# Optimization experiments

Hardware: AMD Instinct MI355X
Metric: run time of the kernel (lower is better)

## Reference

```python
import jax, jax.numpy as jnp
import numpy as np

B, C, P, E, M, H, K = 1024, 8192, 3, 64, 128, 16, 8
SCALE = 0.05
EPS = 1e-12  # tf.math.l2_normalize epsilon


def setup_inputs() -> dict:
    key = jax.random.key(0)
    ks = jax.random.split(key, 16)
    return {
        'pools': jax.random.uniform(ks[0], (B, C), dtype=jnp.float32),            # dense stand-in for SparseTensor batch_pools
        'metapaths': jax.random.uniform(ks[1], (P, C, C), dtype=jnp.float32),     # card-card metapath matrices
        'card_embeddings': jax.random.normal(ks[2], (C, E), dtype=jnp.float32) * SCALE,
        'mp_kernels': jax.random.normal(ks[3], (P, E, M), dtype=jnp.float32) * SCALE,
        'mp_biases': jnp.zeros((P, M, 1), dtype=jnp.float32),
        'Wq': jax.random.normal(ks[4], (M, H, K), dtype=jnp.float32) * SCALE,
        'bq': jnp.zeros((H, K), dtype=jnp.float32),
        'Wk': jax.random.normal(ks[5], (M, H, K), dtype=jnp.float32) * SCALE,
        'bk': jnp.zeros((H, K), dtype=jnp.float32),
        'Wv': jax.random.normal(ks[6], (M, H, K), dtype=jnp.float32) * SCALE,
        'bv': jnp.zeros((H, K), dtype=jnp.float32),
        'Wo': jax.random.normal(ks[7], (H, K, M), dtype=jnp.float32) * SCALE,
        'bo': jnp.zeros((M,), dtype=jnp.float32),
        'pool_kernel': jax.random.normal(ks[8], (M, E), dtype=jnp.float32) * SCALE,
        'pool_bias': jnp.zeros((E,), dtype=jnp.float32),
    }


def _l2_normalize(x, axis):
    # matches tf.math.l2_normalize: x / sqrt(max(sum(x^2), eps))
    sq = jnp.sum(jnp.square(x), axis=axis, keepdims=True)
    return x * jax.lax.rsqrt(jnp.maximum(sq, EPS))


def reference(pools, metapaths, card_embeddings, mp_kernels, mp_biases,
              Wq, bq, Wk, bk, Wv, bv, Wo, bo, pool_kernel, pool_bias):
    # --- MetapathEmbed layers, vectorized over the P metapaths ---
    # path_card_embeddings: act(einsum('ce,em->mc') + bias) -> (P, M, C)
    path_card = jax.nn.silu(jnp.einsum('ce,pem->pmc', card_embeddings, mp_kernels) + mp_biases)
    # path_card_matrix: einsum('mc,cd->dm') -> (P, C, M)
    pcm = jnp.einsum('pmc,pcd->pdm', path_card, metapaths)
    # sparse_dense_matmul(batch_pools, path_card_matrix); stack over metapaths -> (B, P, M)
    x = jnp.einsum('bd,pdm->bpm', pools, pcm)

    # --- keras MultiHeadAttention(query=x, value=x) ---
    q = jnp.einsum('bpm,mhk->bphk', x, Wq) + bq
    k = jnp.einsum('bpm,mhk->bphk', x, Wk) + bk
    v = jnp.einsum('bpm,mhk->bphk', x, Wv) + bv
    scores = jnp.einsum('bphk,bqhk->bhpq', q, k) / np.float32(np.sqrt(K))
    attn = jax.nn.softmax(scores, axis=-1)
    o = jnp.einsum('bhpq,bqhk->bphk', attn, v)
    attended = jnp.einsum('bphk,hkm->bpm', o, Wo) + bo  # (B, P, M)

    # --- pooling head ---
    pre_pool = jnp.sum(attended, axis=1)                       # (B, M)
    pool_embeds = jnp.einsum('bm,me->be', pre_pool, pool_kernel) + pool_bias
    norm_pool = _l2_normalize(pool_embeds, axis=1)             # (B, E)
    norm_cards = _l2_normalize(card_embeddings, axis=1)        # (C, E)
    return (jnp.einsum('be,ce->bc', norm_pool, norm_cards) + 1.0) / 2.0
```

## Files before the change

kernel.cpp:

```cpp
#include <hip/hip_runtime.h>
#include <hip/hip_bf16.h>

typedef unsigned int uint;
typedef unsigned short ushort;
typedef float f32x4 __attribute__((ext_vector_type(4)));
typedef short s16x8 __attribute__((ext_vector_type(8)));
typedef int i32x4 __attribute__((ext_vector_type(4)));
typedef uint u32x2 __attribute__((ext_vector_type(2)));

#define C_DIM 8192
#define B_DIM 1024
#define P_DIM 3
#define E_DIM 64
#define M_DIM 128

#define PCA_OFF   0ull
#define PART_OFF  15728640ull
#define PCMH_OFF  66060288ull
#define PCML_OFF  72351744ull
#define XPART_OFF PART_OFF
#define NPOOL_OFF 78643200ull
#define NCARD_OFF 78774272ull

__device__ __forceinline__ uint bf16_rne(float f) {
  uint u = __builtin_bit_cast(uint, f);
  return (u + 0x7fffu + ((u >> 16) & 1u)) >> 16;
}
__device__ __forceinline__ float bf16_to_f32(uint b) {
  return __builtin_bit_cast(float, b << 16);
}
__device__ __forceinline__ uint pk2(float a, float b) {
  float2 t; t.x = a; t.y = b;
  __hip_bfloat162 h2 = __float22bfloat162_rn(t);
  uint r;
  __builtin_memcpy(&r, &h2, 4);
  return r;
}

__global__ __launch_bounds__(256) void k1_pathcard(
    const float* __restrict__ cardemb, const float* __restrict__ mpk,
    const float* __restrict__ mpbias, ushort* __restrict__ pcA) {
  __shared__ float ce_l[64 * 68];
  const int tid = threadIdx.x;
  const int cb = blockIdx.x;
  const int p  = blockIdx.y;
  for (int r = 0; r < 16; ++r) {
    int i = r * 256 + tid;
    int row = i >> 6, col = i & 63;
    ce_l[row * 68 + col] = cardemb[(size_t)(cb * 64 + row) * 64 + col];
  }
  __syncthreads();
  const int m = tid & 127;
  const int chalf = tid >> 7;
  float kr[64];
#pragma unroll
  for (int e = 0; e < 64; ++e) kr[e] = mpk[(size_t)p * E_DIM * M_DIM + e * M_DIM + m];
  const float bias = mpbias[p * M_DIM + m];
  for (int cl0 = 0; cl0 < 32; ++cl0) {
    int cl = chalf * 32 + cl0;
    float acc = bias;
#pragma unroll
    for (int e = 0; e < 64; ++e) acc += ce_l[cl * 68 + e] * kr[e];
    float s = acc / (1.0f + expf(-acc));
    uint hb = bf16_rne(s);
    uint lb = bf16_rne(s - bf16_to_f32(hb));
    int c = cb * 64 + cl;
    int kt = c >> 5, kl = c & 31;
    size_t off = ((size_t)(p * 256 + kt) * 20480 + (size_t)m * 80 + (size_t)kl * 2) >> 1;
    pcA[off] = (ushort)hb;
    pcA[off + 5120] = (ushort)lb;
  }
}

__global__ __launch_bounds__(256, 3) void k2_big(
    const float* __restrict__ mp, const ushort* __restrict__ pcA,
    float* __restrict__ partial) {
  __shared__ char smem[32768];
  const int tid = threadIdx.x;
  int lin = blockIdx.x + 64 * (blockIdx.y + 4 * blockIdx.z);
  int swz = (lin & 7) * 96 + (lin >> 3);
  const int dt = swz & 63, q = (swz >> 6) & 3, p = swz >> 8;
  const int lane = tid & 63, wid = tid >> 6;
  const int wr = wid >> 1, wc = wid & 1;
  const int r16 = lane & 15, g4 = lane >> 4;
  const float* mpb = mp + (size_t)p * C_DIM * C_DIM + (size_t)dt * 128;
  const char* pcb = (const char*)pcA + (size_t)(p * 256 + q * 64) * 20480;
  const int sd = tid & 127, skh = tid >> 7;
  const int fc = ((sd ^ (sd >> 2)) & 3) << 4;
  const int fr = ((r16 ^ (r16 >> 2)) & 3) << 4;

  f32x4 acc[4][4];
#pragma unroll
  for (int i = 0; i < 4; ++i)
#pragma unroll
    for (int j = 0; j < 4; ++j) acc[i][j] = (f32x4){0.f, 0.f, 0.f, 0.f};

  auto loadB = [&](int t, float* br) {
    int c0 = q * 2048 + t * 32;
#pragma unroll
    for (int ii = 0; ii < 2; ++ii) {
      const float* rp = mpb + (size_t)(c0 + ii * 16 + skh * 8) * C_DIM + sd;
#pragma unroll
      for (int j = 0; j < 8; ++j) br[ii * 8 + j] = rp[(size_t)j * C_DIM];
    }
  };
  auto writeB = [&](const float* br, int buf) {
    char* bb = smem + buf * 16384;
#pragma unroll
    for (int ii = 0; ii < 2; ++ii) {
      uint hw[4], lw[4];
#pragma unroll
      for (int k2 = 0; k2 < 4; ++k2) {
        float v0 = br[ii * 8 + k2 * 2], v1 = br[ii * 8 + k2 * 2 + 1];
        uint h = pk2(v0, v1);
        float h0 = __builtin_bit_cast(float, h << 16);
        float h1 = __builtin_bit_cast(float, h & 0xffff0000u);
        hw[k2] = h;
        lw[k2] = pk2(v0 - h0, v1 - h1);
      }
      int off = sd * 64 + ((((ii * 2 + skh) << 4)) ^ fc);
      *(i32x4*)(bb + off) = (i32x4){(int)hw[0], (int)hw[1], (int)hw[2], (int)hw[3]};
      *(i32x4*)(bb + 8192 + off) = (i32x4){(int)lw[0], (int)lw[1], (int)lw[2], (int)lw[3]};
    }
  };
  auto compute = [&](int t, int buf) {
    const char* At = pcb + (size_t)t * 20480;
    const char* Bb = smem + buf * 16384;
    s16x8 ah[4], al[4], bh[4], bl[4];
#pragma unroll
    for (int i = 0; i < 4; ++i) {
      int off = (wr * 64 + i * 16 + r16) * 80 + g4 * 16;
      ah[i] = *(const s16x8*)(At + off);
      al[i] = *(const s16x8*)(At + 10240 + off);
    }
#pragma unroll
    for (int j = 0; j < 4; ++j) {
      int off = (wc * 64 + j * 16 + r16) * 64 + ((g4 << 4) ^ fr);
      bh[j] = *(const s16x8*)(Bb + off);
      bl[j] = *(const s16x8*)(Bb + 8192 + off);
    }
#pragma unroll
    for (int i = 0; i < 4; ++i)
#pragma unroll
      for (int j = 0; j < 4; ++j) {
        acc[i][j] = __builtin_amdgcn_mfma_f32_16x16x32_bf16(ah[i], bh[j], acc[i][j], 0, 0, 0);
        acc[i][j] = __builtin_amdgcn_mfma_f32_16x16x32_bf16(ah[i], bl[j], acc[i][j], 0, 0, 0);
        acc[i][j] = __builtin_amdgcn_mfma_f32_16x16x32_bf16(al[i], bh[j], acc[i][j], 0, 0, 0);
      }
  };

  float brA[16], brB[16];
  loadB(0, brA);
  loadB(1, brB);
  writeB(brA, 0);
  asm volatile("s_waitcnt lgkmcnt(0)" ::: "memory");
  __builtin_amdgcn_s_barrier();
  __builtin_amdgcn_sched_barrier(0);

#define K2S(T, BRL, BRW, TAIL)                                                \
  {                                                                           \
    if ((T) < 62) loadB((T) + 2, BRL);                                        \
    compute((T), (T) & 1);                                                    \
    if (!(TAIL)) {                                                            \
      writeB(BRW, ((T) + 1) & 1);                                             \
      asm volatile("s_waitcnt lgkmcnt(0)" ::: "memory");                      \
      __builtin_amdgcn_s_barrier();                                           \
      __builtin_amdgcn_sched_barrier(0);                                      \
    }                                                                         \
  }

  for (int t2 = 0; t2 < 32; ++t2) {
    int t = 2 * t2;
    K2S(t, brA, brB, false);
    K2S(t + 1, brB, brA, (t2 == 31));
  }
#undef K2S

  float* part = partial + (size_t)(q * 3 + p) * M_DIM * C_DIM + (size_t)dt * 128;
#pragma unroll
  for (int i = 0; i < 4; ++i)
#pragma unroll
    for (int j = 0; j < 4; ++j)
#pragma unroll
      for (int r = 0; r < 4; ++r)
        part[(size_t)(wr * 64 + i * 16 + g4 * 4 + r) * C_DIM + (wc * 64 + j * 16 + r16)] =
            acc[i][j][r];
}

__global__ __launch_bounds__(256) void k2b_reduce(const float* __restrict__ p0,
                                                  ushort* __restrict__ oh,
                                                  ushort* __restrict__ ol) {
  size_t i = (size_t)blockIdx.x * 256 + threadIdx.x;
  f32x4 a = *(const f32x4*)(p0 + i * 4);
  f32x4 b = *(const f32x4*)(p0 + 3145728ull + i * 4);
  f32x4 c = *(const f32x4*)(p0 + 6291456ull + i * 4);
  f32x4 d = *(const f32x4*)(p0 + 9437184ull + i * 4);
  f32x4 s = (a + b) + (c + d);
  uint h[2], l[2];
#pragma unroll
  for (int k = 0; k < 2; ++k) {
    float v0 = s[k * 2], v1 = s[k * 2 + 1];
    uint hh = pk2(v0, v1);
    float h0 = __builtin_bit_cast(float, hh << 16);
    float h1 = __builtin_bit_cast(float, hh & 0xffff0000u);
    h[k] = hh;
    l[k] = pk2(v0 - h0, v1 - h1);
  }
  *(u32x2*)(oh + i * 4) = (u32x2){h[0], h[1]};
  *(u32x2*)(ol + i * 4) = (u32x2){l[0], l[1]};
}

__global__ __launch_bounds__(256, 2) void k3_x(const float* __restrict__ pools,
                                               const ushort* __restrict__ pcmh,
                                               const ushort* __restrict__ pcml,
                                               float* __restrict__ xpart) {
  const int tid = threadIdx.x;
  const int bt = blockIdx.x, ks = blockIdx.y;
  const int lane = tid & 63, w = tid >> 6;
  const int r16 = lane & 15, g4 = lane >> 4;
  const int rowbase = bt * 32;
  f32x4 acc[2][6];
#pragma unroll
  for (int i = 0; i < 2; ++i)
#pragma unroll
    for (int j = 0; j < 6; ++j) acc[i][j] = (f32x4){0.f, 0.f, 0.f, 0.f};

  f32x4 pv0[2], pv1[2];
#pragma unroll
  for (int i = 0; i < 2; ++i) {
    const float* ap = pools + (size_t)(rowbase + i * 16 + r16) * C_DIM + ks * 512 + g4 * 8;
    pv0[i] = *(const f32x4*)ap;
    pv1[i] = *(const f32x4*)(ap + 4);
  }

  for (int t = 0; t < 16; ++t) {
    int d0 = ks * 512 + t * 32 + g4 * 8;
    s16x8 ah[2], al[2];
#pragma unroll
    for (int i = 0; i < 2; ++i) {
      i32x4 hw, lw;
#pragma unroll
      for (int k2 = 0; k2 < 4; ++k2) {
        float x0 = (k2 < 2) ? pv0[i][k2 * 2] : pv1[i][(k2 - 2) * 2];
        float x1 = (k2 < 2) ? pv0[i][k2 * 2 + 1] : pv1[i][(k2 - 2) * 2 + 1];
        uint h = pk2(x0, x1);
        float h0 = __builtin_bit_cast(float, h << 16);
        float h1 = __builtin_bit_cast(float, h & 0xffff0000u);
        hw[k2] = (int)h;
        lw[k2] = (int)pk2(x0 - h0, x1 - h1);
      }
      ah[i] = __builtin_bit_cast(s16x8, hw);
      al[i] = __builtin_bit_cast(s16x8, lw);
    }
    if (t < 15) {
#pragma unroll
      for (int i = 0; i < 2; ++i) {
        const float* ap =
            pools + (size_t)(rowbase + i * 16 + r16) * C_DIM + d0 + 32;
        pv0[i] = *(const f32x4*)ap;
        pv1[i] = *(const f32x4*)(ap + 4);
      }
    }
#pragma unroll
    for (int j = 0; j < 6; ++j) {
      int col = w * 96 + j * 16 + r16;
      size_t boff = (size_t)col * C_DIM + d0;
      s16x8 bh = *(const s16x8*)(pcmh + boff);
      s16x8 bl = *(const s16x8*)(pcml + boff);
#pragma unroll
      for (int i = 0; i < 2; ++i) {
        acc[i][j] = __builtin_amdgcn_mfma_f32_16x16x32_bf16(ah[i], bh, acc[i][j], 0, 0, 0);
        acc[i][j] = __builtin_amdgcn_mfma_f32_16x16x32_bf16(ah[i], bl, acc[i][j], 0, 0, 0);
        acc[i][j] = __builtin_amdgcn_mfma_f32_16x16x32_bf16(al[i], bh, acc[i][j], 0, 0, 0);
      }
    }
  }
#pragma unroll
  for (int i = 0; i < 2; ++i)
#pragma unroll
    for (int j = 0; j < 6; ++j)
#pragma unroll
      for (int r = 0; r < 4; ++r) {
        int row = rowbase + i * 16 + g4 * 4 + r;
        int col = w * 96 + j * 16 + r16;
        int p = col >> 7, m = col & 127;
        xpart[((size_t)(ks * B_DIM + row) * 3 + p) * M_DIM + m] = acc[i][j][r];
      }
}

__global__ __launch_bounds__(128) void k4_attn(
    const float* __restrict__ xpart, const float* __restrict__ Wq,
    const float* __restrict__ bq, const float* __restrict__ Wk,
    const float* __restrict__ bk, const float* __restrict__ Wv,
    const float* __restrict__ bv, const float* __restrict__ Wo,
    const float* __restrict__ bo, const float* __restrict__ pk,
    const float* __restrict__ pb, ushort* __restrict__ npool) {
  __shared__ float xs[3 * 128], qa[3 * 128], ka[3 * 128], va[3 * 128], oa[3 * 128], pp[128];
  const int t = threadIdx.x;
  const int b = blockIdx.x;
#pragma unroll
  for (int p = 0; p < 3; ++p) {
    float v = 0.f;
    for (int ks = 0; ks < 16; ++ks)
      v += xpart[((size_t)(ks * B_DIM + b) * 3 + p) * M_DIM + t];
    xs[p * 128 + t] = v;
  }
  __syncthreads();
  float qv[3], kv[3], vv[3];
#pragma unroll
  for (int p = 0; p < 3; ++p) { qv[p] = bq[t]; kv[p] = bk[t]; vv[p] = bv[t]; }
  for (int m = 0; m < 128; ++m) {
    float wq = Wq[m * 128 + t], wk = Wk[m * 128 + t], wv = Wv[m * 128 + t];
#pragma unroll
    for (int p = 0; p < 3; ++p) {
      float xv = xs[p * 128 + m];
      qv[p] += xv * wq;
      kv[p] += xv * wk;
      vv[p] += xv * wv;
    }
  }
#pragma unroll
  for (int p = 0; p < 3; ++p) {
    qa[p * 128 + t] = qv[p];
    ka[p * 128 + t] = kv[p];
    va[p * 128 + t] = vv[p];
  }
  __syncthreads();
  const int h = t >> 3;
  float w[3][3];
#pragma unroll
  for (int p = 0; p < 3; ++p) {
    float s[3];
#pragma unroll
    for (int qq = 0; qq < 3; ++qq) {
      float d = 0.f;
#pragma unroll
      for (int kk = 0; kk < 8; ++kk)
        d += qa[p * 128 + h * 8 + kk] * ka[qq * 128 + h * 8 + kk];
      s[qq] = d / 2.8284271247461903f;
    }
    float mx = fmaxf(s[0], fmaxf(s[1], s[2]));
    float e0 = expf(s[0] - mx), e1 = expf(s[1] - mx), e2 = expf(s[2] - mx);
    float inv = 1.0f / (e0 + e1 + e2);
    w[p][0] = e0 * inv; w[p][1] = e1 * inv; w[p][2] = e2 * inv;
  }
#pragma unroll
  for (int p = 0; p < 3; ++p) {
    float o = w[p][0] * va[0 * 128 + t] + w[p][1] * va[1 * 128 + t] + w[p][2] * va[2 * 128 + t];
    oa[p * 128 + t] = o;
  }
  __syncthreads();
  float pre = 3.0f * bo[t];
#pragma unroll
  for (int p = 0; p < 3; ++p)
    for (int hk = 0; hk < 128; ++hk) pre += oa[p * 128 + hk] * Wo[hk * 128 + t];
  pp[t] = pre;
  __syncthreads();
  if (t < 64) {
    float pe = pb[t];
    for (int m = 0; m < 128; ++m) pe += pp[m] * pk[m * 64 + t];
    float ss = pe * pe;
#pragma unroll
    for (int off = 32; off; off >>= 1) ss += __shfl_xor(ss, off, 64);
    float rs = 1.0f / sqrtf(fmaxf(ss, 1e-12f));
    npool[b * 64 + t] = (ushort)bf16_rne(pe * rs);
  }
}

__global__ __launch_bounds__(256) void k4b_ncard(const float* __restrict__ ce,
                                                 ushort* __restrict__ ncard) {
  const int t = threadIdx.x;
  const int r = blockIdx.x * 4 + (t >> 6);
  const int lane = t & 63;
  float v = ce[(size_t)r * 64 + lane];
  float ss = v * v;
#pragma unroll
  for (int off = 32; off; off >>= 1) ss += __shfl_xor(ss, off, 64);
  float rs = 1.0f / sqrtf(fmaxf(ss, 1e-12f));
  ncard[(size_t)r * 64 + lane] = (ushort)bf16_rne(v * rs);
}

__global__ __launch_bounds__(256, 2) void k5_out(const ushort* __restrict__ np_,
                                                 const ushort* __restrict__ nc,
                                                 float* __restrict__ out) {
  const int tid = threadIdx.x;
  const int bt = blockIdx.x, ct = blockIdx.y;
  const int lane = tid & 63, wid = tid >> 6;
  const int wr = wid >> 1, wc = wid & 1;
  const int r16 = lane & 15, g4 = lane >> 4;
  f32x4 acc[4][4];
#pragma unroll
  for (int i = 0; i < 4; ++i)
#pragma unroll
    for (int j = 0; j < 4; ++j) acc[i][j] = (f32x4){0.f, 0.f, 0.f, 0.f};
#pragma unroll
  for (int ks = 0; ks < 2; ++ks) {
    int e0 = ks * 32 + g4 * 8;
    s16x8 af[4], bf_[4];
#pragma unroll
    for (int i = 0; i < 4; ++i)
      af[i] = *(const s16x8*)(np_ + (size_t)(bt * 128 + wr * 64 + i * 16 + r16) * 64 + e0);
#pragma unroll
    for (int j = 0; j < 4; ++j)
      bf_[j] = *(const s16x8*)(nc + (size_t)(ct * 128 + wc * 64 + j * 16 + r16) * 64 + e0);
#pragma unroll
    for (int i = 0; i < 4; ++i)
#pragma unroll
      for (int j = 0; j < 4; ++j)
        acc[i][j] = __builtin_amdgcn_mfma_f32_16x16x32_bf16(af[i], bf_[j], acc[i][j], 0, 0, 0);
  }
#pragma unroll
  for (int i = 0; i < 4; ++i)
#pragma unroll
    for (int j = 0; j < 4; ++j)
#pragma unroll
      for (int r = 0; r < 4; ++r) {
        int row = bt * 128 + wr * 64 + i * 16 + g4 * 4 + r;
        int col = ct * 128 + wc * 64 + j * 16 + r16;
        out[(size_t)row * C_DIM + col] = (acc[i][j][r] + 1.0f) * 0.5f;
      }
}

extern "C" void kernel_launch(void* const* d_in, const int* in_sizes, int n_in,
                              void* d_out, int out_size, void* d_ws, size_t ws_size,
                              hipStream_t stream) {
  const float* pools = (const float*)d_in[0];
  const float* metapaths = (const float*)d_in[1];
  const float* cardemb = (const float*)d_in[2];
  const float* mpk = (const float*)d_in[3];
  const float* mpbias = (const float*)d_in[4];
  const float* Wq = (const float*)d_in[5];
  const float* bq = (const float*)d_in[6];
  const float* Wk = (const float*)d_in[7];
  const float* bk = (const float*)d_in[8];
  const float* Wv = (const float*)d_in[9];
  const float* bv = (const float*)d_in[10];
  const float* Wo = (const float*)d_in[11];
  const float* bo = (const float*)d_in[12];
  const float* pk = (const float*)d_in[13];
  const float* pb = (const float*)d_in[14];
  float* out = (float*)d_out;
  char* ws = (char*)d_ws;

  ushort* pcA = (ushort*)(ws + PCA_OFF);
  float* part = (float*)(ws + PART_OFF);
  ushort* pcmh = (ushort*)(ws + PCMH_OFF);
  ushort* pcml = (ushort*)(ws + PCML_OFF);
  float* xpart = (float*)(ws + XPART_OFF);
  ushort* npool = (ushort*)(ws + NPOOL_OFF);
  ushort* ncard = (ushort*)(ws + NCARD_OFF);

  k1_pathcard<<<dim3(128, 3), dim3(256), 0, stream>>>(cardemb, mpk, mpbias, pcA);
  k2_big<<<dim3(64, 4, 3), dim3(256), 0, stream>>>(metapaths, pcA, part);
  k2b_reduce<<<dim3(3072), dim3(256), 0, stream>>>(part, pcmh, pcml);
  k3_x<<<dim3(32, 16), dim3(256), 0, stream>>>(pools, pcmh, pcml, xpart);
  k4b_ncard<<<dim3(2048), dim3(256), 0, stream>>>(cardemb, ncard);
  k4_attn<<<dim3(1024), dim3(128), 0, stream>>>(xpart, Wq, bq, Wk, bk, Wv, bv, Wo, bo, pk, pb,
                                                npool);
  k5_out<<<dim3(8, 64), dim3(256), 0, stream>>>(npool, ncard, out);
}
```

Before: 384.8 us.

## Double K-tile depth in metapath GEMM to halve barriers per tile

The main metapath GEMM kernel now processes 64 reduction columns per pipeline step instead of 32. This doubles the LDS staging buffers to 64 KB and the register prefetch arrays, and drops occupancy to 2 blocks per CU. B reads now load each fragment once and reuse it across four A rows, and the LDS XOR swizzle changes to an 8-slot pattern to fit the wider rows. The aim is fewer barriers and better latency amortisation per step, at the cost of more registers and less occupancy.

```diff
diff --git a/kernel.cpp b/kernel.cpp
--- a/kernel.cpp
+++ b/kernel.cpp
@@ -72,22 +72,21 @@
   }
 }
 
-__global__ __launch_bounds__(256, 3) void k2_big(
+__global__ __launch_bounds__(256, 2) void k2_big(
     const float* __restrict__ mp, const ushort* __restrict__ pcA,
     float* __restrict__ partial) {
-  __shared__ char smem[32768];
+  __shared__ char smem[65536];
   const int tid = threadIdx.x;
   int lin = blockIdx.x + 64 * (blockIdx.y + 4 * blockIdx.z);
-  int swz = (lin & 7) * 96 + (lin >> 3);
-  const int dt = swz & 63, q = (swz >> 6) & 3, p = swz >> 8;
+  int swzb = (lin & 7) * 96 + (lin >> 3);
+  const int dt = swzb & 63, q = (swzb >> 6) & 3, p = swzb >> 8;
   const int lane = tid & 63, wid = tid >> 6;
   const int wr = wid >> 1, wc = wid & 1;
   const int r16 = lane & 15, g4 = lane >> 4;
   const float* mpb = mp + (size_t)p * C_DIM * C_DIM + (size_t)dt * 128;
   const char* pcb = (const char*)pcA + (size_t)(p * 256 + q * 64) * 20480;
   const int sd = tid & 127, skh = tid >> 7;
-  const int fc = ((sd ^ (sd >> 2)) & 3) << 4;
-  const int fr = ((r16 ^ (r16 >> 2)) & 3) << 4;
+  const int swsd = (sd ^ (sd >> 3)) & 7;
 
   f32x4 acc[4][4];
 #pragma unroll
@@ -95,86 +94,104 @@
 #pragma unroll
     for (int j = 0; j < 4; ++j) acc[i][j] = (f32x4){0.f, 0.f, 0.f, 0.f};
 
-  auto loadB = [&](int t, float* br) {
-    int c0 = q * 2048 + t * 32;
-#pragma unroll
-    for (int ii = 0; ii < 2; ++ii) {
-      const float* rp = mpb + (size_t)(c0 + ii * 16 + skh * 8) * C_DIM + sd;
-#pragma unroll
-      for (int j = 0; j < 8; ++j) br[ii * 8 + j] = rp[(size_t)j * C_DIM];
-    }
-  };
-  auto writeB = [&](const float* br, int buf) {
-    char* bb = smem + buf * 16384;
-#pragma unroll
-    for (int ii = 0; ii < 2; ++ii) {
-      uint hw[4], lw[4];
-#pragma unroll
-      for (int k2 = 0; k2 < 4; ++k2) {
-        float v0 = br[ii * 8 + k2 * 2], v1 = br[ii * 8 + k2 * 2 + 1];
-        uint h = pk2(v0, v1);
-        float h0 = __builtin_bit_cast(float, h << 16);
-        float h1 = __builtin_bit_cast(float, h & 0xffff0000u);
-        hw[k2] = h;
-        lw[k2] = pk2(v0 - h0, v1 - h1);
-      }
-      int off = sd * 64 + ((((ii * 2 + skh) << 4)) ^ fc);
-      *(i32x4*)(bb + off) = (i32x4){(int)hw[0], (int)hw[1], (int)hw[2], (int)hw[3]};
-      *(i32x4*)(bb + 8192 + off) = (i32x4){(int)lw[0], (int)lw[1], (int)lw[2], (int)lw[3]};
-    }
-  };
-  auto compute = [&](int t, int buf) {
-    const char* At = pcb + (size_t)t * 20480;
-    const char* Bb = smem + buf * 16384;
-    s16x8 ah[4], al[4], bh[4], bl[4];
-#pragma unroll
-    for (int i = 0; i < 4; ++i) {
-      int off = (wr * 64 + i * 16 + r16) * 80 + g4 * 16;
-      ah[i] = *(const s16x8*)(At + off);
-      al[i] = *(const s16x8*)(At + 10240 + off);
-    }
-#pragma unroll
-    for (int j = 0; j < 4; ++j) {
-      int off = (wc * 64 + j * 16 + r16) * 64 + ((g4 << 4) ^ fr);
-      bh[j] = *(const s16x8*)(Bb + off);
-      bl[j] = *(const s16x8*)(Bb + 8192 + off);
-    }
-#pragma unroll
-    for (int i = 0; i < 4; ++i)
-#pragma unroll
-      for (int j = 0; j < 4; ++j) {
-        acc[i][j] = __builtin_amdgcn_mfma_f32_16x16x32_bf16(ah[i], bh[j], acc[i][j], 0, 0, 0);
-        acc[i][j] = __builtin_amdgcn_mfma_f32_16x16x32_bf16(ah[i], bl[j], acc[i][j], 0, 0, 0);
-        acc[i][j] = __builtin_amdgcn_mfma_f32_16x16x32_bf16(al[i], bh[j], acc[i][j], 0, 0, 0);
-      }
-  };
-
-  float brA[16], brB[16];
-  loadB(0, brA);
-  loadB(1, brB);
-  writeB(brA, 0);
+  float brA[32], brB[32];
+  s16x8 ah[2][4], al[2][4];
+
+#define LOADB(T, BR)                                                          \
+  {                                                                           \
+    int c0_ = q * 2048 + (T) * 64;                                            \
+    _Pragma("unroll") for (int ii = 0; ii < 4; ++ii) {                        \
+      const float* rp_ = mpb + (size_t)(c0_ + ii * 16 + skh * 8) * C_DIM + sd;\
+      _Pragma("unroll") for (int j = 0; j < 8; ++j)                           \
+          BR[ii * 8 + j] = rp_[(size_t)j * C_DIM];                            \
+    }                                                                         \
+  }
+
+#define WRITEB(BR, BUF)                                                       \
+  {                                                                           \
+    char* bb_ = smem + (BUF) * 32768;                                         \
+    _Pragma("unroll") for (int ii = 0; ii < 4; ++ii) {                        \
+      uint hw_[4], lw_[4];                                                    \
+      _Pragma("unroll") for (int k2 = 0; k2 < 4; ++k2) {                      \
+        float v0_ = BR[ii * 8 + k2 * 2], v1_ = BR[ii * 8 + k2 * 2 + 1];       \
+        uint h_ = pk2(v0_, v1_);                                              \
+        float h0_ = __builtin_bit_cast(float, h_ << 16);                      \
+        float h1_ = __builtin_bit_cast(float, h_ & 0xffff0000u);              \
+        hw_[k2] = h_;                                                         \
+        lw_[k2] = pk2(v0_ - h0_, v1_ - h1_);                                  \
+      }                                                                       \
+      int off_ = sd * 128 + ((((ii * 2 + skh) ^ swsd)) << 4);                 \
+      *(i32x4*)(bb_ + off_) =                                                 \
+          (i32x4){(int)hw_[0], (int)hw_[1], (int)hw_[2], (int)hw_[3]};        \
+      *(i32x4*)(bb_ + 16384 + off_) =                                         \
+          (i32x4){(int)lw_[0], (int)lw_[1], (int)lw_[2], (int)lw_[3]};        \
+    }                                                                         \
+  }
+
+#define LOADA(T)                                                              \
+  {                                                                           \
+    _Pragma("unroll") for (int s = 0; s < 2; ++s) {                           \
+      const char* At_ = pcb + (size_t)(2 * (T) + s) * 20480;                  \
+      _Pragma("unroll") for (int i = 0; i < 4; ++i) {                         \
+        int off_ = (wr * 64 + i * 16 + r16) * 80 + g4 * 16;                   \
+        ah[s][i] = *(const s16x8*)(At_ + off_);                               \
+        al[s][i] = *(const s16x8*)(At_ + 10240 + off_);                       \
+      }                                                                       \
+    }                                                                         \
+  }
+
+#define MFMAS(BUF)                                                            \
+  {                                                                           \
+    const char* Bb_ = smem + (BUF) * 32768;                                   \
+    _Pragma("unroll") for (int s = 0; s < 2; ++s) {                           \
+      _Pragma("unroll") for (int j = 0; j < 4; ++j) {                         \
+        int col_ = wc * 64 + j * 16 + r16;                                    \
+        int slot_ = (s * 4 + g4) ^ ((col_ ^ (col_ >> 3)) & 7);                \
+        int off_ = col_ * 128 + (slot_ << 4);                                 \
+        s16x8 bh_ = *(const s16x8*)(Bb_ + off_);                              \
+        s16x8 bl_ = *(const s16x8*)(Bb_ + 16384 + off_);                      \
+        _Pragma("unroll") for (int i = 0; i < 4; ++i) {                       \
+          acc[i][j] =                                                         \
+              __builtin_amdgcn_mfma_f32_16x16x32_bf16(ah[s][i], bh_, acc[i][j], 0, 0, 0); \
+          acc[i][j] =                                                         \
+              __builtin_amdgcn_mfma_f32_16x16x32_bf16(ah[s][i], bl_, acc[i][j], 0, 0, 0); \
+          acc[i][j] =                                                         \
+              __builtin_amdgcn_mfma_f32_16x16x32_bf16(al[s][i], bh_, acc[i][j], 0, 0, 0); \
+        }                                                                     \
+      }                                                                       \
+    }                                                                         \
+  }
+
+  LOADB(0, brA);
+  LOADB(1, brB);
+  WRITEB(brA, 0);
   asm volatile("s_waitcnt lgkmcnt(0)" ::: "memory");
   __builtin_amdgcn_s_barrier();
   __builtin_amdgcn_sched_barrier(0);
 
-#define K2S(T, BRL, BRW, TAIL)                                                \
+#define K2STEP(T, BRL, BRW)                                                   \
   {                                                                           \
-    if ((T) < 62) loadB((T) + 2, BRL);                                        \
-    compute((T), (T) & 1);                                                    \
-    if (!(TAIL)) {                                                            \
-      writeB(BRW, ((T) + 1) & 1);                                             \
+    LOADA(T);                                                                 \
+    if ((T) + 2 < 32) LOADB((T) + 2, BRL);                                    \
+    MFMAS((T) & 1);                                                           \
+    if ((T) < 31) {                                                           \
+      WRITEB(BRW, ((T) + 1) & 1);                                             \
       asm volatile("s_waitcnt lgkmcnt(0)" ::: "memory");                      \
       __builtin_amdgcn_s_barrier();                                           \
       __builtin_amdgcn_sched_barrier(0);                                      \
     }                                                                         \
   }
 
-  for (int t2 = 0; t2 < 32; ++t2) {
+  for (int t2 = 0; t2 < 16; ++t2) {
     int t = 2 * t2;
-    K2S(t, brA, brB, false);
-    K2S(t + 1, brB, brA, (t2 == 31));
-  }
-#undef K2S
+    K2STEP(t, brA, brB);
+    K2STEP(t + 1, brB, brA);
+  }
+#undef K2STEP
+#undef MFMAS
+#undef LOADA
+#undef WRITEB
+#undef LOADB
 
   float* part = partial + (size_t)(q * 3 + p) * M_DIM * C_DIM + (size_t)dt * 128;
 #pragma unroll
```

Measured after the change: 443.1 us. 15.1% more time.
